# Performance work log

Measured on AMD Instinct MI355X. Metric: run time of the kernel, lower is better.

## Reference

```python
import jax, jax.numpy as jnp
import numpy as np

B, N, C = 1, 2048, 1024
H, D = 16, 64          # num_heads, head_dim
S = 8                  # number of frames; tokens per frame = N // S
NEG_INF = jnp.float32(-1e30)  # stand-in for -inf, numerically safe under jit


def setup_inputs() -> dict:
    key = jax.random.key(0)
    ks = jax.random.split(key, 8)
    x = jax.random.normal(ks[0], (B, N, C), dtype=jnp.float32)
    # tokens grouped contiguously by frame (sorted frame ids)
    frame_ids = jnp.repeat(jnp.arange(S, dtype=jnp.int32), N // S)
    is_hub = jax.random.bernoulli(ks[1], 0.05, (N,))
    adj = jax.random.bernoulli(ks[2], 0.25, (S, S))
    adj = adj.at[jnp.arange(S), jnp.arange(S)].set(True)  # frames always see self
    frame_bias = jax.random.normal(ks[3], (S, S), dtype=jnp.float32) * 0.1
    Wqkv = jax.random.normal(ks[4], (C, 3 * C), dtype=jnp.float32) * 0.02
    bqkv = jnp.zeros((3 * C,), dtype=jnp.float32)
    Wproj = jax.random.normal(ks[5], (C, C), dtype=jnp.float32) * 0.02
    bproj = jnp.zeros((C,), dtype=jnp.float32)
    return {"x": x, "frame_ids": frame_ids, "is_hub": is_hub, "adj": adj,
            "frame_bias": frame_bias, "Wqkv": Wqkv, "bqkv": bqkv,
            "Wproj": Wproj, "bproj": bproj}


def reference(x, frame_ids, is_hub, adj, frame_bias, Wqkv, bqkv, Wproj, bproj):
    # qkv projection: (B,N,3C) -> (3,B,H,N,D)
    qkv = (x @ Wqkv + bqkv).reshape(B, N, 3, H, D).transpose(2, 0, 3, 1, 4)
    q, k, v = qkv[0], qkv[1], qkv[2]

    # flex_attention: scores scaled by 1/sqrt(D) BEFORE score_mod
    scores = jnp.einsum("bhnd,bhmd->bhnm", q, k) * (D ** -0.5)

    # score_mod, vectorized over all (qi,kj) pairs:
    fi = frame_ids                                   # (N,)
    allow = adj[fi][:, fi]                           # (N,N) frame adjacency per token pair
    diff_frame = fi[:, None] != fi[None, :]
    hub_block = diff_frame & (is_hub[:, None] | is_hub[None, :])
    allow = allow & ~hub_block                       # mask_hub_tokens=True
    bias = frame_bias[fi][:, fi]                     # soft_mask=True: add frame-level bias

    scores = jnp.where(allow, scores + bias, NEG_INF)  # broadcast over (b,h)
    attn = jax.nn.softmax(scores, axis=-1)
    out = jnp.einsum("bhnm,bhmd->bhnd", attn, v)
    out = out.transpose(0, 2, 1, 3).reshape(B, N, C)
    return out @ Wproj + bproj
```

## Files before the change

### kernel.cpp

```cpp
#include <hip/hip_runtime.h>

#define NTOK 2048
#define CDIM 1024
#define NHEAD 16
#define HDIM 64
#define NFRM 8
#define FTOK 256

typedef unsigned short ushort;
typedef unsigned long long u64;
typedef __attribute__((ext_vector_type(8))) short short8;
typedef __attribute__((ext_vector_type(8))) ushort ushort8;
typedef __attribute__((ext_vector_type(4))) ushort ushort4v;
typedef __attribute__((ext_vector_type(4))) float floatx4;

__device__ __forceinline__ ushort f2bf(float f) {
    unsigned int u = __float_as_uint(f);
    return (ushort)((u + 0x7fffu + ((u >> 16) & 1u)) >> 16);
}

__device__ __forceinline__ unsigned int cvt_pk_bf16(float lo, float hi) {
    unsigned int r;
    asm volatile("v_cvt_pk_bf16_f32 %0, %1, %2" : "=v"(r) : "v"(lo), "v"(hi));
    return r;
}

__device__ __forceinline__ void gload_lds16(const void* g, void* l) {
    __builtin_amdgcn_global_load_lds(
        (const __attribute__((address_space(1))) unsigned int*)(uintptr_t)g,
        (__attribute__((address_space(3))) unsigned int*)(unsigned int)(uintptr_t)l,
        16, 0, 0);
}


__global__ __launch_bounds__(256)
void prep_kernel(const float* __restrict__ x, ushort* __restrict__ xb,
                 const float* __restrict__ Wqkv, ushort* __restrict__ wqkvT,
                 const float* __restrict__ Wproj, ushort* __restrict__ wprojT,
                 const int* __restrict__ is_hub, u64* __restrict__ hubmask)
{
    __shared__ ushort LT[64][72];
    const int b = blockIdx.x, t = threadIdx.x;

    if (b < 2048) {
        int i = b * 256 + t;
        int tok = i >> 8, c0 = (i & 255) * 4;
        float4 f = ((const float4*)x)[i];
        ushort4v o = { f2bf(f.x), f2bf(f.y), f2bf(f.z), f2bf(f.w) };
        size_t idx = ((size_t)((tok >> 6) * 32 + (c0 >> 5)) << 11)
                   + ((((tok & 63) >> 4) * 4 + ((c0 >> 3) & 3)) << 7)
                   + ((tok & 15) << 3) + (c0 & 7);
        *(ushort4v*)&xb[idx] = o;
        return;
    }
    if (b >= 3072) {
        if (t < NTOK / 64) {
            u64 m = 0;
            for (int j = 0; j < 64; ++j)
                m |= (u64)(is_hub[t * 64 + j] != 0) << j;
            hubmask[t] = m;
        }
        return;
    }

    const float* W; ushort* WT; int K, N, n0, k0;
    if (b < 2816) { int idx = b - 2048; W = Wqkv;  WT = wqkvT;  K = 1024; N = 3072;
                    n0 = (idx % 48) * 64; k0 = (idx / 48) * 64; }
    else          { int idx = b - 2816; W = Wproj; WT = wprojT; K = 1024; N = 1024;
                    n0 = (idx & 15) * 64; k0 = (idx >> 4) * 64; }

    const int kr = t >> 4, nc = t & 15;
#pragma unroll
    for (int i = 0; i < 4; ++i) {
        int k = kr + i * 16;
        float4 w4 = *(const float4*)(W + (size_t)(k0 + k) * N + n0 + nc * 4);
        LT[nc*4+0][k] = f2bf(w4.x);
        LT[nc*4+1][k] = f2bf(w4.y);
        LT[nc*4+2][k] = f2bf(w4.z);
        LT[nc*4+3][k] = f2bf(w4.w);
    }
    __syncthreads();
    const int n = t >> 2;
#pragma unroll
    for (int half = 0; half < 2; ++half) {
        int kc = (t & 3) + 4 * half;
        ushort8 v = *(const ushort8*)&LT[n][kc * 8];
        *(ushort8*)(WT + (size_t)(n0 + n) * K + k0 + kc * 8) = v;
    }
}

template<int BM>
__global__ __launch_bounds__(256)
void gemm_bt_kernel(const ushort* __restrict__ Afrag, const ushort* __restrict__ BT,
                    const float* __restrict__ bias, void* __restrict__ out,
                    ushort* __restrict__ vtb,
                    int M, int N, int K, int mode)
{
    constexpr int MI = BM / 32;
    __shared__ ushort Bs[2][128 * 64];

    const int t = threadIdx.x;
    const int wave = t >> 6, lane = t & 63;
    const int quad = lane >> 4, l15 = lane & 15;
    const int row0 = blockIdx.y * BM, col0 = blockIdx.x * 128;
    const int wm = (wave >> 1) * (BM / 2), wn = (wave & 1) * 64;

    const int rb = wave * 32;
    const int srb = lane >> 3;
    const int scb = (((lane & 7) ^ (srb & 7)) << 3);

    const int absRow = row0 + wm;
    const int rowtile = absRow >> 6;
    const int ibase = (absRow & 63) >> 4;
    const ushort* Abase = Afrag + ((size_t)rowtile * 32 << 11) + lane * 8;

    floatx4 acc[MI][4];
#pragma unroll
    for (int i = 0; i < MI; ++i)
#pragma unroll
        for (int j = 0; j < 4; ++j) acc[i][j] = (floatx4){0.f, 0.f, 0.f, 0.f};

    const int NPH = K >> 6;
    short8 a0[MI], a1[MI], an0[MI], an1[MI];

#pragma unroll
    for (int ii = 0; ii < 4; ++ii)
        gload_lds16(BT + (size_t)(col0 + rb + ii * 8 + srb) * K + scb,
                    &Bs[0][(rb + ii * 8) * 64]);
#pragma unroll
    for (int i = 0; i < MI; ++i) {
        a0[i] = *(const short8*)(Abase + ((size_t)0 << 11) + ((ibase + i) << 9));
        a1[i] = *(const short8*)(Abase + ((size_t)1 << 11) + ((ibase + i) << 9));
    }

    for (int p = 0; p < NPH; ++p) {
        __syncthreads();
        if (p + 1 < NPH) {
            const int nb = (p + 1) & 1;
#pragma unroll
            for (int ii = 0; ii < 4; ++ii)
                gload_lds16(BT + (size_t)(col0 + rb + ii * 8 + srb) * K + (p + 1) * 64 + scb,
                            &Bs[nb][(rb + ii * 8) * 64]);
#pragma unroll
            for (int i = 0; i < MI; ++i) {
                an0[i] = *(const short8*)(Abase + ((size_t)(2 * p + 2) << 11) + ((ibase + i) << 9));
                an1[i] = *(const short8*)(Abase + ((size_t)(2 * p + 3) << 11) + ((ibase + i) << 9));
            }
        }
        const ushort* bs = Bs[p & 1];
        const int swz = (l15 & 7) << 3;

        short8 bfr[4];
#pragma unroll
        for (int j = 0; j < 4; ++j)
            bfr[j] = *(const short8*)&bs[(((wn + j * 16 + l15) * 64) + quad * 8) ^ swz];
#pragma unroll
        for (int i = 0; i < MI; ++i)
#pragma unroll
            for (int j = 0; j < 4; ++j)
                acc[i][j] = __builtin_amdgcn_mfma_f32_16x16x32_bf16(a0[i], bfr[j], acc[i][j], 0, 0, 0);
#pragma unroll
        for (int j = 0; j < 4; ++j)
            bfr[j] = *(const short8*)&bs[(((wn + j * 16 + l15) * 64) + 32 + quad * 8) ^ swz];
#pragma unroll
        for (int i = 0; i < MI; ++i)
#pragma unroll
            for (int j = 0; j < 4; ++j)
                acc[i][j] = __builtin_amdgcn_mfma_f32_16x16x32_bf16(a1[i], bfr[j], acc[i][j], 0, 0, 0);

#pragma unroll
        for (int i = 0; i < MI; ++i) { a0[i] = an0[i]; a1[i] = an1[i]; }
    }

    if (mode == 0) {
        float* outf = (float*)out;
#pragma unroll
        for (int j = 0; j < 4; ++j) {
            int col = col0 + wn + j * 16 + l15;
            float bb = bias[col];
#pragma unroll
            for (int i = 0; i < MI; ++i) {
                int rowb = row0 + wm + i * 16 + quad * 4;
#pragma unroll
                for (int r = 0; r < 4; ++r)
                    outf[(size_t)(rowb + r) * N + col] = acc[i][j][r] + bb;
            }
        }
    } else {
        ushort* outb = (ushort*)out;
#pragma unroll
        for (int j = 0; j < 4; ++j) {
            int col = col0 + wn + j * 16 + l15;
            float bb = bias[col];
            int part = col >> 10, hh = (col >> 6) & 15, d = col & 63;
            if (part < 2) {
                int half = d >> 5, qk = (d & 31) >> 3, elem = d & 7;
                ushort* base = outb + (size_t)(part * NHEAD + hh) * (NTOK * HDIM);
#pragma unroll
                for (int i = 0; i < MI; ++i) {
                    int rowb = row0 + wm + i * 16 + quad * 4;
#pragma unroll
                    for (int r = 0; r < 4; ++r) {
                        int tok = rowb + r;
                        int tile = tok >> 6, kk = tok & 63;
                        int nt = kk >> 4, lk = kk & 15;
                        base[(size_t)tile * 4096 + ((nt * 2 + half) * 64 + qk * 16 + lk) * 8 + elem]
                            = f2bf(acc[i][j][r] + bb);
                    }
                }
            } else {
                int dt = d >> 4, lv = d & 15;
                ushort* base = vtb + (size_t)hh * (NTOK * HDIM);
#pragma unroll
                for (int i = 0; i < MI; ++i) {
                    int rowb = row0 + wm + i * 16 + quad * 4;
                    int tile = rowb >> 6, kk = rowb & 63;
                    int bslot = ((kk & 15) << 2) | (kk >> 4);
#pragma unroll
                    for (int r = 0; r < 4; ++r) {
                        int s = bslot + 4 * r;
                        int off = ((dt * 2 + (s >> 5)) * 64 + ((s >> 3) & 3) * 16 + lv) * 8 + (s & 7);
                        base[(size_t)tile * 4096 + off] = f2bf(acc[i][j][r] + bb);
                    }
                }
            }
        }
    }
}

__global__ __launch_bounds__(512, 4)
void attn_tile_kernel(const ushort* __restrict__ qkvb,
                      const ushort* __restrict__ vTb,
                      const int* __restrict__ frame_ids,
                      const u64* __restrict__ hubmask,
                      const int* __restrict__ adj,
                      const float* __restrict__ frame_bias,
                      ushort* __restrict__ attnb)
{
    __shared__ ushort Ps[8][16 * 72];
    __shared__ float  Om[4][64][21];

    const int t = threadIdx.x;
    const int wave = t >> 6, lane = t & 63;
    const int wq = wave & 3, wk = wave >> 2;
    const int quad = lane >> 4, l15 = lane & 15;
    const int b = blockIdx.x;
    const int h = b & 15, q0 = (b >> 4) * 64;

    const ushort* Qh = qkvb + (size_t)h * (NTOK * HDIM);
    const ushort* Kh = qkvb + (size_t)(NHEAD + h) * (NTOK * HDIM);
    const ushort* Vh = vTb + (size_t)h * (NTOK * HDIM);

    const ushort* qt = Qh + (size_t)(q0 >> 6) * 4096;
    short8 aq0 = *(const short8*)(qt + ((wq * 2 + 0) * 64 + lane) * 8);
    short8 aq1 = *(const short8*)(qt + ((wq * 2 + 1) * 64 + lane) * 8);

    const int fq = frame_ids[q0];
    unsigned vpack = 0; int nv = 0;
#pragma unroll
    for (int f = 0; f < NFRM; ++f)
        if (adj[fq * NFRM + f]) { vpack |= (unsigned)f << (3 * nv); ++nv; }

    const u64 hmq = hubmask[q0 >> 6];
    int qh[4];
#pragma unroll
    for (int r = 0; r < 4; ++r) qh[r] = (int)((hmq >> (wq * 16 + quad * 4 + r)) & 1);

    float lpart[4] = {0.f, 0.f, 0.f, 0.f};
    floatx4 oacc[4];
#pragma unroll
    for (int dt = 0; dt < 4; ++dt) oacc[dt] = (floatx4){0.f, 0.f, 0.f, 0.f};

    const float C1 = 0.18033688011112042f;
    const float L2E = 1.4426950408889634f;

    const int nmine = nv * 2;
    int vt = wk;
    for (int j = 0; j < nmine; ++j, vt += 2) {
        const int fj = (int)((vpack >> (3 * (vt >> 2))) & 7u);
        const int k0 = fj * FTOK + (vt & 3) * 64;
        const float fbl = frame_bias[fq * NFRM + fj] * L2E;
        const bool same = (fj == fq);
        const u64 hmk = hubmask[k0 >> 6];

        const ushort* kt = Kh + (size_t)(k0 >> 6) * 4096;
        const ushort* vtp = Vh + (size_t)(k0 >> 6) * 4096;
        short8 kf[8], vf[8];
#pragma unroll
        for (int idx = 0; idx < 8; ++idx)
            kf[idx] = *(const short8*)(kt + (idx * 64 + lane) * 8);
#pragma unroll
        for (int idx = 0; idx < 8; ++idx)
            vf[idx] = *(const short8*)(vtp + (idx * 64 + lane) * 8);

        floatx4 s[4];
#pragma unroll
        for (int nt = 0; nt < 4; ++nt)
            s[nt] = (floatx4){0.f, 0.f, 0.f, 0.f};
        __builtin_amdgcn_s_setprio(1);
#pragma unroll
        for (int nt = 0; nt < 4; ++nt) {
            s[nt] = __builtin_amdgcn_mfma_f32_16x16x32_bf16(aq0, kf[2*nt],     s[nt], 0, 0, 0);
            s[nt] = __builtin_amdgcn_mfma_f32_16x16x32_bf16(aq1, kf[2*nt + 1], s[nt], 0, 0, 0);
        }
        __builtin_amdgcn_s_setprio(0);

        float mkf[4];
#pragma unroll
        for (int nt = 0; nt < 4; ++nt) {
            int kb = (int)(((unsigned)(hmk >> (nt * 16)) >> l15) & 1u);
            mkf[nt] = (same || !kb) ? 1.f : 0.f;
        }
        float mrf[4];
#pragma unroll
        for (int r = 0; r < 4; ++r) mrf[r] = (same || !qh[r]) ? 1.f : 0.f;

#pragma unroll
        for (int r = 0; r < 4; ++r) {
            float pv[4];
#pragma unroll
            for (int nt = 0; nt < 4; ++nt) {
                float e = __builtin_amdgcn_exp2f(fmaf(s[nt][r], C1, fbl));
                pv[nt] = e * mkf[nt] * mrf[r];
            }
            lpart[r] += (pv[0] + pv[1]) + (pv[2] + pv[3]);
            uint2 pk;
            pk.x = cvt_pk_bf16(pv[0], pv[1]);
            pk.y = cvt_pk_bf16(pv[2], pv[3]);
            *(uint2*)&Ps[wave][(quad * 4 + r) * 72 + l15 * 4] = pk;
        }

        short8 ap0 = *(const short8*)&Ps[wave][l15 * 72 + quad * 8];
        short8 ap1 = *(const short8*)&Ps[wave][l15 * 72 + 32 + quad * 8];
        __builtin_amdgcn_s_setprio(1);
#pragma unroll
        for (int dt = 0; dt < 4; ++dt) {
            oacc[dt] = __builtin_amdgcn_mfma_f32_16x16x32_bf16(ap0, vf[2*dt],     oacc[dt], 0, 0, 0);
            oacc[dt] = __builtin_amdgcn_mfma_f32_16x16x32_bf16(ap1, vf[2*dt + 1], oacc[dt], 0, 0, 0);
        }
        __builtin_amdgcn_s_setprio(0);
    }

    if (wk == 1) {
#pragma unroll
        for (int dt = 0; dt < 4; ++dt)
#pragma unroll
            for (int r = 0; r < 4; ++r) Om[wq][lane][dt * 4 + r] = oacc[dt][r];
#pragma unroll
        for (int r = 0; r < 4; ++r) Om[wq][lane][16 + r] = lpart[r];
    }
    __syncthreads();
    if (wk == 1) return;

#pragma unroll
    for (int dt = 0; dt < 4; ++dt)
#pragma unroll
        for (int r = 0; r < 4; ++r) oacc[dt][r] += Om[wq][lane][dt * 4 + r];
#pragma unroll
    for (int r = 0; r < 4; ++r) lpart[r] += Om[wq][lane][16 + r];

    float linv[4];
#pragma unroll
    for (int r = 0; r < 4; ++r) {
        float ls = lpart[r];
        ls += __shfl_xor(ls, 1);
        ls += __shfl_xor(ls, 2);
        ls += __shfl_xor(ls, 4);
        ls += __shfl_xor(ls, 8);
        linv[r] = 1.0f / ls;
    }

    const size_t tbase = ((size_t)(q0 >> 6) * 32) << 11;
#pragma unroll
    for (int dt = 0; dt < 4; ++dt) {
        size_t kbase = tbase + ((size_t)(h * 2 + (dt >> 1)) << 11)
                     + ((wq * 4 + (dt & 1) * 2 + (l15 >> 3)) << 7)
                     + (quad << 5) + (l15 & 7);
#pragma unroll
        for (int r = 0; r < 4; ++r)
            attnb[kbase + r * 8] = f2bf(oacc[dt][r] * linv[r]);
    }
}

extern "C" void kernel_launch(void* const* d_in, const int* in_sizes, int n_in,
                              void* d_out, int out_size, void* d_ws, size_t ws_size,
                              hipStream_t stream)
{
    const float* x          = (const float*)d_in[0];
    const int*   frame_ids  = (const int*)d_in[1];
    const int*   is_hub     = (const int*)d_in[2];
    const int*   adj        = (const int*)d_in[3];
    const float* frame_bias = (const float*)d_in[4];
    const float* Wqkv       = (const float*)d_in[5];
    const float* bqkv       = (const float*)d_in[6];
    const float* Wproj      = (const float*)d_in[7];
    const float* bproj      = (const float*)d_in[8];
    float* out = (float*)d_out;

    ushort* xb     = (ushort*)d_ws;
    ushort* wqkvT  = xb     + 2097152;
    ushort* wprojT = wqkvT  + 3145728;
    ushort* qkvb   = wprojT + 1048576;
    ushort* vTb    = qkvb   + 6291456;
    ushort* attnb  = vTb    + 2097152;
    u64*    hubmask = (u64*)(attnb + 2097152);

    prep_kernel<<<dim3(3073), dim3(256), 0, stream>>>(
        x, xb, Wqkv, wqkvT, Wproj, wprojT, is_hub, hubmask);

    gemm_bt_kernel<128><<<dim3(3 * CDIM / 128, NTOK / 128), dim3(256), 0, stream>>>(
        xb, wqkvT, bqkv, qkvb, vTb, NTOK, 3 * CDIM, CDIM, 1);

    attn_tile_kernel<<<dim3(512), dim3(512), 0, stream>>>(
        qkvb, vTb, frame_ids, hubmask, adj, frame_bias, attnb);

    gemm_bt_kernel<64><<<dim3(CDIM / 128, NTOK / 64), dim3(256), 0, stream>>>(
        attnb, wprojT, bproj, out, nullptr, NTOK, CDIM, CDIM, 0);
}
```

Measured before the change: 140.0 us.

## Double-buffer K/V register tiles in attention loop and relax launch bounds

The attention inner loop now prefetches the next K/V tile into a second register buffer while computing on the current one, which hides global load latency behind the MFMA and exp work. Launch bounds go from 4 to 2 blocks per SM so the compiler has room for the extra registers. The cost is lower occupancy, and that lost occupancy may offset the overlap. Each wave's tile count (nv*2) is always even, so the unroll by two stays correct.

```diff
diff --git a/kernel.cpp b/kernel.cpp
--- a/kernel.cpp
+++ b/kernel.cpp
@@ -228,7 +228,7 @@
     }
 }
 
-__global__ __launch_bounds__(512, 4)
+__global__ __launch_bounds__(512, 2)
 void attn_tile_kernel(const ushort* __restrict__ qkvb,
                       const ushort* __restrict__ vTb,
                       const int* __restrict__ frame_ids,
@@ -275,71 +275,81 @@
     const float L2E = 1.4426950408889634f;
 
     const int nmine = nv * 2;
-    int vt = wk;
-    for (int j = 0; j < nmine; ++j, vt += 2) {
-        const int fj = (int)((vpack >> (3 * (vt >> 2))) & 7u);
-        const int k0 = fj * FTOK + (vt & 3) * 64;
-        const float fbl = frame_bias[fq * NFRM + fj] * L2E;
-        const bool same = (fj == fq);
-        const u64 hmk = hubmask[k0 >> 6];
-
-        const ushort* kt = Kh + (size_t)(k0 >> 6) * 4096;
-        const ushort* vtp = Vh + (size_t)(k0 >> 6) * 4096;
-        short8 kf[8], vf[8];
-#pragma unroll
-        for (int idx = 0; idx < 8; ++idx)
-            kf[idx] = *(const short8*)(kt + (idx * 64 + lane) * 8);
-#pragma unroll
-        for (int idx = 0; idx < 8; ++idx)
-            vf[idx] = *(const short8*)(vtp + (idx * 64 + lane) * 8);
-
-        floatx4 s[4];
-#pragma unroll
-        for (int nt = 0; nt < 4; ++nt)
-            s[nt] = (floatx4){0.f, 0.f, 0.f, 0.f};
-        __builtin_amdgcn_s_setprio(1);
-#pragma unroll
-        for (int nt = 0; nt < 4; ++nt) {
-            s[nt] = __builtin_amdgcn_mfma_f32_16x16x32_bf16(aq0, kf[2*nt],     s[nt], 0, 0, 0);
-            s[nt] = __builtin_amdgcn_mfma_f32_16x16x32_bf16(aq1, kf[2*nt + 1], s[nt], 0, 0, 0);
-        }
-        __builtin_amdgcn_s_setprio(0);
-
-        float mkf[4];
-#pragma unroll
-        for (int nt = 0; nt < 4; ++nt) {
-            int kb = (int)(((unsigned)(hmk >> (nt * 16)) >> l15) & 1u);
-            mkf[nt] = (same || !kb) ? 1.f : 0.f;
-        }
-        float mrf[4];
-#pragma unroll
-        for (int r = 0; r < 4; ++r) mrf[r] = (same || !qh[r]) ? 1.f : 0.f;
-
-#pragma unroll
-        for (int r = 0; r < 4; ++r) {
-            float pv[4];
-#pragma unroll
-            for (int nt = 0; nt < 4; ++nt) {
-                float e = __builtin_amdgcn_exp2f(fmaf(s[nt][r], C1, fbl));
-                pv[nt] = e * mkf[nt] * mrf[r];
-            }
-            lpart[r] += (pv[0] + pv[1]) + (pv[2] + pv[3]);
-            uint2 pk;
-            pk.x = cvt_pk_bf16(pv[0], pv[1]);
-            pk.y = cvt_pk_bf16(pv[2], pv[3]);
-            *(uint2*)&Ps[wave][(quad * 4 + r) * 72 + l15 * 4] = pk;
-        }
-
-        short8 ap0 = *(const short8*)&Ps[wave][l15 * 72 + quad * 8];
-        short8 ap1 = *(const short8*)&Ps[wave][l15 * 72 + 32 + quad * 8];
-        __builtin_amdgcn_s_setprio(1);
-#pragma unroll
-        for (int dt = 0; dt < 4; ++dt) {
-            oacc[dt] = __builtin_amdgcn_mfma_f32_16x16x32_bf16(ap0, vf[2*dt],     oacc[dt], 0, 0, 0);
-            oacc[dt] = __builtin_amdgcn_mfma_f32_16x16x32_bf16(ap1, vf[2*dt + 1], oacc[dt], 0, 0, 0);
-        }
-        __builtin_amdgcn_s_setprio(0);
-    }
+    short8 kA[8], vA[8], kB[8], vB[8];
+
+#define LOADKV(VT, KF, VF) do {                                               \
+        const int fj_ = (int)((vpack >> (3 * ((VT) >> 2))) & 7u);             \
+        const int k0_ = fj_ * FTOK + ((VT) & 3) * 64;                         \
+        const ushort* kt_ = Kh + (size_t)(k0_ >> 6) * 4096;                   \
+        const ushort* vp_ = Vh + (size_t)(k0_ >> 6) * 4096;                   \
+        _Pragma("unroll")                                                     \
+        for (int i_ = 0; i_ < 8; ++i_)                                        \
+            KF[i_] = *(const short8*)(kt_ + (i_ * 64 + lane) * 8);            \
+        _Pragma("unroll")                                                     \
+        for (int i_ = 0; i_ < 8; ++i_)                                        \
+            VF[i_] = *(const short8*)(vp_ + (i_ * 64 + lane) * 8);            \
+    } while (0)
+
+#define TILE_BODY(VT, KF, VF) do {                                            \
+        const int fj_ = (int)((vpack >> (3 * ((VT) >> 2))) & 7u);             \
+        const int k0_ = fj_ * FTOK + ((VT) & 3) * 64;                         \
+        const float fbl_ = frame_bias[fq * NFRM + fj_] * L2E;                 \
+        const bool same_ = (fj_ == fq);                                       \
+        const u64 hmk_ = hubmask[k0_ >> 6];                                   \
+        floatx4 s_[4];                                                        \
+        _Pragma("unroll")                                                     \
+        for (int nt = 0; nt < 4; ++nt) s_[nt] = (floatx4){0.f, 0.f, 0.f, 0.f};\
+        __builtin_amdgcn_s_setprio(1);                                        \
+        _Pragma("unroll")                                                     \
+        for (int nt = 0; nt < 4; ++nt) {                                      \
+            s_[nt] = __builtin_amdgcn_mfma_f32_16x16x32_bf16(aq0, KF[2*nt],     s_[nt], 0, 0, 0); \
+            s_[nt] = __builtin_amdgcn_mfma_f32_16x16x32_bf16(aq1, KF[2*nt + 1], s_[nt], 0, 0, 0); \
+        }                                                                     \
+        __builtin_amdgcn_s_setprio(0);                                        \
+        float mkf_[4];                                                        \
+        _Pragma("unroll")                                                     \
+        for (int nt = 0; nt < 4; ++nt) {                                      \
+            int kb_ = (int)(((unsigned)(hmk_ >> (nt * 16)) >> l15) & 1u);     \
+            mkf_[nt] = (same_ || !kb_) ? 1.f : 0.f;                           \
+        }                                                                     \
+        float mrf_[4];                                                        \
+        _Pragma("unroll")                                                     \
+        for (int r = 0; r < 4; ++r) mrf_[r] = (same_ || !qh[r]) ? 1.f : 0.f;  \
+        _Pragma("unroll")                                                     \
+        for (int r = 0; r < 4; ++r) {                                         \
+            float pv_[4];                                                     \
+            _Pragma("unroll")                                                 \
+            for (int nt = 0; nt < 4; ++nt) {                                  \
+                float e_ = __builtin_amdgcn_exp2f(fmaf(s_[nt][r], C1, fbl_)); \
+                pv_[nt] = e_ * mkf_[nt] * mrf_[r];                            \
+            }                                                                 \
+            lpart[r] += (pv_[0] + pv_[1]) + (pv_[2] + pv_[3]);                \
+            uint2 pk_;                                                        \
+            pk_.x = cvt_pk_bf16(pv_[0], pv_[1]);                              \
+            pk_.y = cvt_pk_bf16(pv_[2], pv_[3]);                              \
+            *(uint2*)&Ps[wave][(quad * 4 + r) * 72 + l15 * 4] = pk_;          \
+        }                                                                     \
+        short8 ap0_ = *(const short8*)&Ps[wave][l15 * 72 + quad * 8];         \
+        short8 ap1_ = *(const short8*)&Ps[wave][l15 * 72 + 32 + quad * 8];    \
+        __builtin_amdgcn_s_setprio(1);                                        \
+        _Pragma("unroll")                                                     \
+        for (int dt = 0; dt < 4; ++dt) {                                      \
+            oacc[dt] = __builtin_amdgcn_mfma_f32_16x16x32_bf16(ap0_, VF[2*dt],     oacc[dt], 0, 0, 0); \
+            oacc[dt] = __builtin_amdgcn_mfma_f32_16x16x32_bf16(ap1_, VF[2*dt + 1], oacc[dt], 0, 0, 0); \
+        }                                                                     \
+        __builtin_amdgcn_s_setprio(0);                                        \
+    } while (0)
+
+    LOADKV(wk, kA, vA);
+    for (int m = 0; m < nmine; m += 2) {
+        const int vt0 = wk + 2 * m;
+        LOADKV(vt0 + 2, kB, vB);
+        TILE_BODY(vt0, kA, vA);
+        if (m + 2 < nmine) LOADKV(vt0 + 4, kA, vA);
+        TILE_BODY(vt0 + 2, kB, vB);
+    }
+#undef LOADKV
+#undef TILE_BODY
 
     if (wk == 1) {
 #pragma unroll
```

After: 146.3 us. 1.05x slower.
